# Optimization experiments

Hardware: AMD Instinct MI355X
Metric: run time of the kernel (lower is better)

## Reference

```python
import jax, jax.numpy as jnp
import numpy as np

DIM_M = 512
NEG_INF = -1e30


def setup_inputs() -> dict:
    key = jax.random.key(0)
    k1, k2, k3, k4, k5, k6, k7 = jax.random.split(key, 7)
    B, Lc, Lq, d = 16, 1024, 512, DIM_M
    C = jax.random.normal(k1, (B, Lc, d), dtype=jnp.float32)
    Q = jax.random.normal(k2, (B, Lq, d), dtype=jnp.float32)
    cmask = jax.random.randint(k3, (B, Lc), 0, 2).astype(jnp.float32)
    qmask = jax.random.randint(k4, (B, Lq), 0, 2).astype(jnp.float32)
    lim = np.sqrt(1.0 / d)
    w = jax.random.uniform(k5, (3 * d,), minval=-lim, maxval=lim, dtype=jnp.float32)
    # out_linear: Linear(4d -> d), torch default init
    bound = np.sqrt(1.0 / (4 * d))
    out_w = jax.random.uniform(k6, (d, 4 * d), minval=-bound, maxval=bound, dtype=jnp.float32)
    out_b = jax.random.uniform(k7, (d,), minval=-bound, maxval=bound, dtype=jnp.float32)
    return {"C": C, "Q": Q, "cmask": cmask, "qmask": qmask, "w": w, "out_w": out_w, "out_b": out_b}


def _mask_logits(t, m):
    return t * m + (1.0 - m) * NEG_INF


def reference(C, Q, cmask, qmask, w, out_w, out_b):
    d = C.shape[-1]
    w1, w2, w3 = w[:d], w[d:2 * d], w[2 * d:]
    # Decomposed trilinear similarity (same math as cat([Ct,Qt,Ct*Qt]) @ w):
    # S[b,i,j] = C[b,i]@w1 + Q[b,j]@w2 + (C[b,i]*w3) @ Q[b,j]
    S = (C @ w1)[:, :, None] + (Q @ w2)[:, None, :] \
        + jnp.einsum('bid,bjd->bij', C * w3, Q)  # [B, Lc, Lq]
    qm = qmask[:, None, :]  # [B, 1, Lq]
    cm = cmask[:, :, None]  # [B, Lc, 1]
    S1 = jax.nn.softmax(_mask_logits(S, qm), axis=2)  # over Lq
    S2 = jax.nn.softmax(_mask_logits(S, cm), axis=1)  # over Lc
    A = jnp.einsum('bij,bjd->bid', S1, Q)  # [B, Lc, d]
    # bmm(bmm(S1, S2^T), C) == S1 @ (S2^T @ C) by associativity (cheaper)
    S2TC = jnp.einsum('bij,bid->bjd', S2, C)  # [B, Lq, d]
    Bm = jnp.einsum('bij,bjd->bid', S1, S2TC)  # [B, Lc, d]
    out = jnp.concatenate([C, A, C * A, C * Bm], axis=2)  # [B, Lc, 4d]
    # dropout inactive (inference); out_linear
    return out @ out_w.T + out_b
```

## Files before the change

### kernel.cpp

```cpp
#include <hip/hip_runtime.h>
#include <hip/hip_bf16.h>


#define NB 16
#define LC 1024
#define LQ 512
#define DM 512
#define D4 2048
#define NEGINF (-1e30f)
#define LDA64 72
#define LDA32 40

typedef __bf16 v8bf __attribute__((ext_vector_type(8)));
typedef __bf16 v4bf __attribute__((ext_vector_type(4)));
typedef float  v4f  __attribute__((ext_vector_type(4)));

#define MFMA16 __builtin_amdgcn_mfma_f32_16x16x32_bf16

#define TILE_SETUP8 \
  const int t = threadIdx.x, lane = t & 63, wave = t >> 6; \
  const int wm = wave >> 2, wn = wave & 3, quad = lane >> 4, col = lane & 15; \
  const int sr = t >> 2;

#define ZERO_ACC8 \
  v4f acc[4][2]; \
  _Pragma("unroll") for (int x = 0; x < 4; ++x) \
  _Pragma("unroll") for (int y = 0; y < 2; ++y) \
  _Pragma("unroll") for (int r = 0; r < 4; ++r) acc[x][y][r] = 0.f;

#define FRAG_MMA8S(AL, BL, LDA, KO) do { \
  v8bf af_[4], bf_[2]; \
  _Pragma("unroll") for (int x = 0; x < 4; ++x) \
    af_[x] = *(const v8bf*)&AL[(wm * 64 + x * 16 + col) * LDA + KO + quad * 8]; \
  _Pragma("unroll") for (int y = 0; y < 2; ++y) \
    bf_[y] = *(const v8bf*)&BL[(wn * 32 + y * 16 + col) * LDA + KO + quad * 8]; \
  _Pragma("unroll") for (int x = 0; x < 4; ++x) \
  _Pragma("unroll") for (int y = 0; y < 2; ++y) \
    acc[x][y] = MFMA16(af_[x], bf_[y], acc[x][y], 0, 0, 0); \
} while (0)

__device__ __forceinline__ void xcd_remap(int& bx, int& by, int& bz) {
  const int gx = gridDim.x, gy = gridDim.y, gz = gridDim.z;
  int flat = bx + gx * (by + gy * bz);
  int per = (gx * gy * gz) >> 3;
  int nw = (flat & 7) * per + (flat >> 3);
  bx = nw % gx;
  int r = nw / gx;
  by = r % gy;
  bz = r / gy;
}

__device__ __forceinline__ v8bf cvt8f(float4 a, float4 b) {
  v8bf h;
  h[0] = (__bf16)a.x; h[1] = (__bf16)a.y; h[2] = (__bf16)a.z; h[3] = (__bf16)a.w;
  h[4] = (__bf16)b.x; h[5] = (__bf16)b.y; h[6] = (__bf16)b.z; h[7] = (__bf16)b.w;
  return h;
}

__global__ void k_rowdots(const float* __restrict__ C, const float* __restrict__ Q,
                          const float* __restrict__ w,
                          float* __restrict__ cw1, float* __restrict__ qw2) {
  const int wid = threadIdx.x >> 6, lane = threadIdx.x & 63;
  const int row = blockIdx.x * 4 + wid;
  const bool isC = row < NB * LC;
  const float* src = isC ? (C + (size_t)row * DM) : (Q + (size_t)(row - NB * LC) * DM);
  const float* wv  = isC ? w : (w + DM);
  float v = 0.f;
#pragma unroll
  for (int tt = 0; tt < 8; ++tt) {
    int k = lane + 64 * tt;
    v += src[k] * wv[k];
  }
#pragma unroll
  for (int off = 32; off; off >>= 1) v += __shfl_down(v, off, 64);
  if (lane == 0) {
    if (isC) cw1[row] = v;
    else     qw2[row - NB * LC] = v;
  }
}

__global__ void k_transpose(const float* __restrict__ in, __bf16* __restrict__ outT,
                            int R, int Cd) {
  __shared__ __bf16 tile[64][66];
  const int b = blockIdx.z;
  const int r0 = blockIdx.y * 64, c0 = blockIdx.x * 64;
  const int tr = threadIdx.x >> 6, tc = threadIdx.x & 63;
  const float* inb = in + (size_t)b * R * Cd;
  __bf16* outb = outT + (size_t)b * Cd * R;
  for (int r = tr; r < 64; r += 4)
    tile[r][tc] = (__bf16)inb[(size_t)(r0 + r) * Cd + c0 + tc];
  __syncthreads();
  for (int c = tr; c < 64; c += 4)
    outb[(size_t)(c0 + c) * R + r0 + tc] = tile[tc][c];
}

__global__ void k_owcvt(const float* __restrict__ OW, __bf16* __restrict__ OWb) {
  size_t i = ((size_t)blockIdx.x * 256 + threadIdx.x) * 4;
  float4 f = *(const float4*)(OW + i);
  v4bf h; h[0] = (__bf16)f.x; h[1] = (__bf16)f.y; h[2] = (__bf16)f.z; h[3] = (__bf16)f.w;
  *(v4bf*)(OWb + i) = h;
}

__global__ __launch_bounds__(512) void k_mfma_S(
    const float* __restrict__ C, const float* __restrict__ Q, const float* __restrict__ w,
    const float* __restrict__ cw1, const float* __restrict__ qw2, float* __restrict__ S) {
  __shared__ __bf16 Al[128 * LDA64], Bl[128 * LDA64];
  int bx = blockIdx.x, by = blockIdx.y, bz = blockIdx.z;
  xcd_remap(bx, by, bz);
  const int b = bz, i0 = by * 128, j0 = bx * 128;
  TILE_SETUP8
  const int skc = (t & 3) * 16;
  const float* Cb = C + (size_t)b * LC * DM;
  const float* Qb = Q + (size_t)b * LQ * DM;
  const float* w3 = w + 2 * DM;
  float4 pc[4], pq[4];
  auto load = [&](int k0) {
    const float* ca = Cb + (size_t)(i0 + sr) * DM + k0 + skc;
    const float* qa = Qb + (size_t)(j0 + sr) * DM + k0 + skc;
#pragma unroll
    for (int u = 0; u < 4; ++u) {
      pc[u] = *(const float4*)(ca + 4 * u);
      pq[u] = *(const float4*)(qa + 4 * u);
    }
  };
  load(0);
  ZERO_ACC8
  for (int k0 = 0; k0 < DM; k0 += 64) {
    const float* wa = w3 + k0 + skc;
#pragma unroll
    for (int u = 0; u < 2; ++u) {
      float4 c0 = pc[2 * u], c1 = pc[2 * u + 1];
      float4 w0 = *(const float4*)(wa + 8 * u), w1 = *(const float4*)(wa + 8 * u + 4);
      v8bf ah;
      ah[0] = (__bf16)(c0.x * w0.x); ah[1] = (__bf16)(c0.y * w0.y);
      ah[2] = (__bf16)(c0.z * w0.z); ah[3] = (__bf16)(c0.w * w0.w);
      ah[4] = (__bf16)(c1.x * w1.x); ah[5] = (__bf16)(c1.y * w1.y);
      ah[6] = (__bf16)(c1.z * w1.z); ah[7] = (__bf16)(c1.w * w1.w);
      *(v8bf*)&Al[sr * LDA64 + skc + 8 * u] = ah;
      *(v8bf*)&Bl[sr * LDA64 + skc + 8 * u] = cvt8f(pq[2 * u], pq[2 * u + 1]);
    }
    __syncthreads();
    int kn = k0 + 64; if (kn >= DM) kn = 0;
    load(kn);
    FRAG_MMA8S(Al, Bl, LDA64, 0);
    FRAG_MMA8S(Al, Bl, LDA64, 32);
    __syncthreads();
  }
  float* Sb = S + (size_t)b * LC * LQ;
#pragma unroll
  for (int x = 0; x < 4; ++x) {
    const int mB = i0 + wm * 64 + x * 16 + quad * 4;
    float cv[4];
#pragma unroll
    for (int r = 0; r < 4; ++r) cv[r] = cw1[b * LC + mB + r];
#pragma unroll
    for (int y = 0; y < 2; ++y) {
      const int j = j0 + wn * 32 + y * 16 + col;
      const float qv = qw2[b * LQ + j];
#pragma unroll
      for (int r = 0; r < 4; ++r)
        Sb[(size_t)(mB + r) * LQ + j] = acc[x][y][r] + cv[r] + qv;
    }
  }
}

__global__ __launch_bounds__(1024) void k_softstat(
    const float* __restrict__ S, const float* __restrict__ qmask,
    const float* __restrict__ cmask, __bf16* __restrict__ S1,
    float2* __restrict__ pstat) {
  __shared__ float2 cst[16][LQ];
  const int b = blockIdx.y, ic = blockIdx.x;
  const int tid = threadIdx.x, wv = tid >> 6, lane = tid & 63;
  const float* qm  = qmask + b * LQ;
  const float* cm  = cmask + b * LC + ic * 64;
  const float* Sb  = S  + ((size_t)b * LC + ic * 64) * LQ;
  __bf16*      S1b = S1 + ((size_t)b * LC + ic * 64) * LQ;
  float colm[8], cols[8];
#pragma unroll
  for (int tt = 0; tt < 8; ++tt) { colm[tt] = -3e38f; cols[tt] = 0.f; }
  for (int it = 0; it < 4; ++it) {
    const int r = wv * 4 + it;
    const float cmv = cm[r];
    const float* Srow = Sb + (size_t)r * LQ;
    float sv[8], l1[8];
    float m = -3e38f;
#pragma unroll
    for (int tt = 0; tt < 8; ++tt) {
      int j = lane + 64 * tt;
      sv[tt] = Srow[j];
      float qv = qm[j];
      l1[tt] = qv * sv[tt] + (1.f - qv) * NEGINF;
      m = fmaxf(m, l1[tt]);
    }
#pragma unroll
    for (int off = 32; off; off >>= 1) m = fmaxf(m, __shfl_xor(m, off, 64));
    float e[8], s = 0.f;
#pragma unroll
    for (int tt = 0; tt < 8; ++tt) { e[tt] = __expf(l1[tt] - m); s += e[tt]; }
#pragma unroll
    for (int off = 32; off; off >>= 1) s += __shfl_xor(s, off, 64);
    const float inv = 1.f / s;
#pragma unroll
    for (int tt = 0; tt < 8; ++tt)
      S1b[(size_t)r * LQ + lane + 64 * tt] = (__bf16)(e[tt] * inv);
#pragma unroll
    for (int tt = 0; tt < 8; ++tt) {
      float l2 = cmv * sv[tt] + (1.f - cmv) * NEGINF;
      if (l2 > colm[tt]) { cols[tt] *= __expf(colm[tt] - l2); colm[tt] = l2; }
      cols[tt] += __expf(l2 - colm[tt]);
    }
  }
#pragma unroll
  for (int tt = 0; tt < 8; ++tt) cst[wv][lane + 64 * tt] = make_float2(colm[tt], cols[tt]);
  __syncthreads();
  if (tid < LQ) {
    float M = -3e38f, Sd = 0.f;
#pragma unroll
    for (int k = 0; k < 16; ++k) {
      float2 p = cst[k][tid];
      float nM = fmaxf(M, p.x);
      Sd = Sd * __expf(M - nM) + p.y * __expf(p.x - nM);
      M = nM;
    }
    pstat[((size_t)(b * 16 + ic) * LQ) + tid] = make_float2(M, Sd);
  }
}

__global__ void k_colwrite(const float* __restrict__ S, const float* __restrict__ cmask,
                           const float2* __restrict__ pstat, __bf16* __restrict__ S2T) {
  __shared__ float Mf[64], If[64];
  __shared__ __bf16 tile[64][66];
  const int b = blockIdx.z, ic = blockIdx.y, j0 = blockIdx.x * 64;
  const int c = threadIdx.x & 63, ip = threadIdx.x >> 6;
  if (threadIdx.x < 64) {
    float M = -3e38f, Sd = 0.f;
#pragma unroll
    for (int k = 0; k < 16; ++k) {
      float2 p = pstat[((size_t)(b * 16 + k) * LQ) + j0 + threadIdx.x];
      float nM = fmaxf(M, p.x);
      Sd = Sd * __expf(M - nM) + p.y * __expf(p.x - nM);
      M = nM;
    }
    Mf[threadIdx.x] = M; If[threadIdx.x] = 1.f / Sd;
  }
  __syncthreads();
  const float M = Mf[c], inv = If[c];
  const float* Sb = S + ((size_t)b * LC + ic * 64) * LQ;
  const float* cm = cmask + b * LC + ic * 64;
  for (int r = ip; r < 64; r += 4) {
    float mk = cm[r];
    float logit = mk * Sb[(size_t)r * LQ + j0 + c] + (1.f - mk) * NEGINF;
    tile[r][c] = (__bf16)(__expf(logit - M) * inv);
  }
  __syncthreads();
  __bf16* S2Tb = S2T + ((size_t)b * LQ + j0) * LC + ic * 64;
  for (int jr = ip; jr < 64; jr += 4)
    S2Tb[(size_t)jr * LC + c] = tile[c][jr];
}

__global__ __launch_bounds__(512) void k_mfma_A(
    const __bf16* __restrict__ S1, const __bf16* __restrict__ QT, __bf16* __restrict__ Aw) {
  __shared__ __bf16 Al[128 * LDA64], Bl[128 * LDA64];
  int bx = blockIdx.x, by = blockIdx.y, bz = blockIdx.z;
  xcd_remap(bx, by, bz);
  const int b = bz, i0 = by * 128, n0 = bx * 128;
  TILE_SETUP8
  const int skc = (t & 3) * 16;
  const __bf16* Ar = S1 + (size_t)b * LC * LQ + (size_t)(i0 + sr) * LQ + skc;
  const __bf16* Br = QT + (size_t)b * DM * LQ + (size_t)(n0 + sr) * LQ + skc;
  v8bf pa0, pa1, pb0, pb1;
  auto load = [&](int k0) {
    pa0 = *(const v8bf*)(Ar + k0); pa1 = *(const v8bf*)(Ar + k0 + 8);
    pb0 = *(const v8bf*)(Br + k0); pb1 = *(const v8bf*)(Br + k0 + 8);
  };
  load(0);
  ZERO_ACC8
  for (int k0 = 0; k0 < LQ; k0 += 64) {
    *(v8bf*)&Al[sr * LDA64 + skc] = pa0; *(v8bf*)&Al[sr * LDA64 + skc + 8] = pa1;
    *(v8bf*)&Bl[sr * LDA64 + skc] = pb0; *(v8bf*)&Bl[sr * LDA64 + skc + 8] = pb1;
    __syncthreads();
    int kn = k0 + 64; if (kn >= LQ) kn = 0;
    load(kn);
    FRAG_MMA8S(Al, Bl, LDA64, 0);
    FRAG_MMA8S(Al, Bl, LDA64, 32);
    __syncthreads();
  }
  __bf16* Ab = Aw + (size_t)b * LC * DM;
#pragma unroll
  for (int x = 0; x < 4; ++x) {
    const int mB = i0 + wm * 64 + x * 16 + quad * 4;
#pragma unroll
    for (int y = 0; y < 2; ++y) {
      const int n = n0 + wn * 32 + y * 16 + col;
#pragma unroll
      for (int r = 0; r < 4; ++r)
        Ab[(size_t)(mB + r) * DM + n] = (__bf16)acc[x][y][r];
    }
  }
}

__global__ __launch_bounds__(512) void k_mfma_T(
    const __bf16* __restrict__ S2T, const __bf16* __restrict__ CT, __bf16* __restrict__ S2TCT) {
  __shared__ __bf16 Al[128 * LDA64], Bl[128 * LDA64];
  int bx = blockIdx.x, by = blockIdx.y, bz = blockIdx.z;
  xcd_remap(bx, by, bz);
  const int b = bz, j0 = by * 128, n0 = bx * 128;
  TILE_SETUP8
  const int skc = (t & 3) * 16;
  const __bf16* Ar = S2T + (size_t)b * LQ * LC + (size_t)(j0 + sr) * LC + skc;
  const __bf16* Br = CT  + (size_t)b * DM * LC + (size_t)(n0 + sr) * LC + skc;
  v8bf pa0, pa1, pb0, pb1;
  auto load = [&](int k0) {
    pa0 = *(const v8bf*)(Ar + k0); pa1 = *(const v8bf*)(Ar + k0 + 8);
    pb0 = *(const v8bf*)(Br + k0); pb1 = *(const v8bf*)(Br + k0 + 8);
  };
  load(0);
  ZERO_ACC8
  for (int k0 = 0; k0 < LC; k0 += 64) {
    *(v8bf*)&Al[sr * LDA64 + skc] = pa0; *(v8bf*)&Al[sr * LDA64 + skc + 8] = pa1;
    *(v8bf*)&Bl[sr * LDA64 + skc] = pb0; *(v8bf*)&Bl[sr * LDA64 + skc + 8] = pb1;
    __syncthreads();
    int kn = k0 + 64; if (kn >= LC) kn = 0;
    load(kn);
    FRAG_MMA8S(Al, Bl, LDA64, 0);
    FRAG_MMA8S(Al, Bl, LDA64, 32);
    __syncthreads();
  }
#pragma unroll
  for (int x = 0; x < 4; ++x) {
    const int jB = j0 + wm * 64 + x * 16 + quad * 4;
#pragma unroll
    for (int y = 0; y < 2; ++y) {
      const int n = n0 + wn * 32 + y * 16 + col;
      v4bf h;
#pragma unroll
      for (int r = 0; r < 4; ++r) h[r] = (__bf16)acc[x][y][r];
      *(v4bf*)&S2TCT[((size_t)b * DM + n) * LQ + jB] = h;
    }
  }
}

__global__ __launch_bounds__(512) void k_mfma_Bm(
    const __bf16* __restrict__ S1, const __bf16* __restrict__ S2TCT, __bf16* __restrict__ Bmw) {
  __shared__ __bf16 Al[128 * LDA64], Bl[128 * LDA64];
  int bx = blockIdx.x, by = blockIdx.y, bz = blockIdx.z;
  xcd_remap(bx, by, bz);
  const int b = bz, i0 = by * 128, n0 = bx * 128;
  TILE_SETUP8
  const int skc = (t & 3) * 16;
  const __bf16* Ar = S1    + (size_t)b * LC * LQ + (size_t)(i0 + sr) * LQ + skc;
  const __bf16* Br = S2TCT + (size_t)b * DM * LQ + (size_t)(n0 + sr) * LQ + skc;
  v8bf pa0, pa1, pb0, pb1;
  auto load = [&](int k0) {
    pa0 = *(const v8bf*)(Ar + k0); pa1 = *(const v8bf*)(Ar + k0 + 8);
    pb0 = *(const v8bf*)(Br + k0); pb1 = *(const v8bf*)(Br + k0 + 8);
  };
  load(0);
  ZERO_ACC8
  for (int k0 = 0; k0 < LQ; k0 += 64) {
    *(v8bf*)&Al[sr * LDA64 + skc] = pa0; *(v8bf*)&Al[sr * LDA64 + skc + 8] = pa1;
    *(v8bf*)&Bl[sr * LDA64 + skc] = pb0; *(v8bf*)&Bl[sr * LDA64 + skc + 8] = pb1;
    __syncthreads();
    int kn = k0 + 64; if (kn >= LQ) kn = 0;
    load(kn);
    FRAG_MMA8S(Al, Bl, LDA64, 0);
    FRAG_MMA8S(Al, Bl, LDA64, 32);
    __syncthreads();
  }
  __bf16* Bb = Bmw + (size_t)b * LC * DM;
#pragma unroll
  for (int x = 0; x < 4; ++x) {
    const int mB = i0 + wm * 64 + x * 16 + quad * 4;
#pragma unroll
    for (int y = 0; y < 2; ++y) {
      const int n = n0 + wn * 32 + y * 16 + col;
#pragma unroll
      for (int r = 0; r < 4; ++r)
        Bb[(size_t)(mB + r) * DM + n] = (__bf16)acc[x][y][r];
    }
  }
}

__global__ __launch_bounds__(512) void k_mfma_out(
    const float* __restrict__ C, const __bf16* __restrict__ Aw, const __bf16* __restrict__ Bmw,
    const __bf16* __restrict__ OWb, const float* __restrict__ ob, float* __restrict__ out) {
  __shared__ __bf16 Asg[4][128 * LDA32], Bsg[4][128 * LDA32];
  int bx = blockIdx.x, by = blockIdx.y, bz = blockIdx.z;
  xcd_remap(bx, by, bz);
  const int b = bz, i0 = by * 128, n0 = bx * 128;
  TILE_SETUP8
  const int skc = (t & 3) * 8;
  const float*  Cr = C   + (size_t)b * LC * DM + (size_t)(i0 + sr) * DM + skc;
  const __bf16* Ar = Aw  + (size_t)b * LC * DM + (size_t)(i0 + sr) * DM + skc;
  const __bf16* Br = Bmw + (size_t)b * LC * DM + (size_t)(i0 + sr) * DM + skc;
  const __bf16* Wr = OWb + (size_t)(n0 + sr) * D4 + skc;
  float4 pc0, pc1; v8bf pA, pB, pw[4];
  auto load = [&](int kl) {
    pc0 = *(const float4*)(Cr + kl); pc1 = *(const float4*)(Cr + kl + 4);
    pA = *(const v8bf*)(Ar + kl);
    pB = *(const v8bf*)(Br + kl);
#pragma unroll
    for (int s = 0; s < 4; ++s) pw[s] = *(const v8bf*)(Wr + s * DM + kl);
  };
  load(0);
  ZERO_ACC8
  for (int kl = 0; kl < DM; kl += 32) {
    float cf[8] = {pc0.x, pc0.y, pc0.z, pc0.w, pc1.x, pc1.y, pc1.z, pc1.w};
    v8bf hC, hCA, hCB;
#pragma unroll
    for (int e = 0; e < 8; ++e) {
      hC[e]  = (__bf16)cf[e];
      hCA[e] = (__bf16)(cf[e] * (float)pA[e]);
      hCB[e] = (__bf16)(cf[e] * (float)pB[e]);
    }
    const int off = sr * LDA32 + skc;
    *(v8bf*)&Asg[0][off] = hC;
    *(v8bf*)&Asg[1][off] = pA;
    *(v8bf*)&Asg[2][off] = hCA;
    *(v8bf*)&Asg[3][off] = hCB;
#pragma unroll
    for (int s = 0; s < 4; ++s) *(v8bf*)&Bsg[s][off] = pw[s];
    __syncthreads();
    int kn = kl + 32; if (kn >= DM) kn = 0;
    load(kn);
#pragma unroll
    for (int s = 0; s < 4; ++s) FRAG_MMA8S(Asg[s], Bsg[s], LDA32, 0);
    __syncthreads();
  }
  float* outb = out + (size_t)b * LC * DM;
#pragma unroll
  for (int x = 0; x < 4; ++x) {
    const int mB = i0 + wm * 64 + x * 16 + quad * 4;
#pragma unroll
    for (int y = 0; y < 2; ++y) {
      const int n = n0 + wn * 32 + y * 16 + col;
      const float bv = ob[n];
#pragma unroll
      for (int r = 0; r < 4; ++r)
        outb[(size_t)(mB + r) * DM + n] = acc[x][y][r] + bv;
    }
  }
}

extern "C" void kernel_launch(void* const* d_in, const int* in_sizes, int n_in,
                              void* d_out, int out_size, void* d_ws, size_t ws_size,
                              hipStream_t stream) {
  const float* C     = (const float*)d_in[0];
  const float* Q     = (const float*)d_in[1];
  const float* cmask = (const float*)d_in[2];
  const float* qmask = (const float*)d_in[3];
  const float* w     = (const float*)d_in[4];
  const float* out_w = (const float*)d_in[5];
  const float* out_b = (const float*)d_in[6];
  float* out = (float*)d_out;

  char* base = (char*)d_ws;
  float*  cw1   = (float*)base;
  float*  qw2   = (float*)(base + 65536);
  char*   R     = base + 131072;
  float*  S     = (float*)R;
  __bf16* Aw    = (__bf16*)R;
  __bf16* CT    = (__bf16*)(R + (16u << 20));
  __bf16* Bmw   = (__bf16*)(R + (16u << 20));
  __bf16* S1    = (__bf16*)(base + 131072 + (32u << 20));
  __bf16* S2T   = (__bf16*)(base + 131072 + (48u << 20));
  __bf16* OWbf  = S2T;
  char*   Z     = base + 131072 + (64u << 20);
  float2* pstat = (float2*)Z;
  __bf16* QT    = (__bf16*)Z;
  __bf16* S2TCT = (__bf16*)Z;
  (void)in_sizes; (void)n_in; (void)out_size; (void)ws_size;

  k_rowdots<<<(NB * LC + NB * LQ) / 4, 256, 0, stream>>>(C, Q, w, cw1, qw2);
  k_mfma_S<<<dim3(LQ / 128, LC / 128, NB), 512, 0, stream>>>(C, Q, w, cw1, qw2, S);
  k_softstat<<<dim3(LC / 64, NB), 1024, 0, stream>>>(S, qmask, cmask, S1, pstat);
  k_colwrite<<<dim3(LQ / 64, LC / 64, NB), 256, 0, stream>>>(S, cmask, pstat, S2T);
  k_transpose<<<dim3(DM / 64, LQ / 64, NB), 256, 0, stream>>>(Q, QT, LQ, DM);
  k_transpose<<<dim3(DM / 64, LC / 64, NB), 256, 0, stream>>>(C, CT, LC, DM);
  k_mfma_A<<<dim3(DM / 128, LC / 128, NB), 512, 0, stream>>>(S1, QT, Aw);
  k_mfma_T<<<dim3(DM / 128, LQ / 128, NB), 512, 0, stream>>>(S2T, CT, S2TCT);
  k_owcvt<<<DM * D4 / 1024, 256, 0, stream>>>(out_w, OWbf);
  k_mfma_Bm<<<dim3(DM / 128, LC / 128, NB), 512, 0, stream>>>(S1, S2TCT, Bmw);
  k_mfma_out<<<dim3(DM / 128, LC / 128, NB), 512, 0, stream>>>(C, Aw, Bmw, OWbf, out_b, out);
}
```

Baseline: 281.1 us.

## Fuse row dots into S GEMM, vectorize softmax/transpose, use 4-wave 64x64 warp tiles

Removes the separate row-dot kernel by computing C·w1 and Q·w2 inside the S GEMM's load loop and reducing them through shared memory. Vectorizes global loads and stores in softstat, colwrite and transpose (float4 reads, packed bf16 writes). Switches the A, Bm and output GEMMs from 8 waves with 64x32 per-wave tiles to 4 waves with 64x64 per-wave tiles, which raises register use per thread and changes occupancy. The fused dot products add redundant w1/w2 loads per block of the S GEMM.

```diff
diff --git a/kernel.cpp b/kernel.cpp
--- a/kernel.cpp
+++ b/kernel.cpp
@@ -19,8 +19,7 @@
 
 #define TILE_SETUP8 \
   const int t = threadIdx.x, lane = t & 63, wave = t >> 6; \
-  const int wm = wave >> 2, wn = wave & 3, quad = lane >> 4, col = lane & 15; \
-  const int sr = t >> 2;
+  const int wm = wave >> 2, wn = wave & 3, quad = lane >> 4, col = lane & 15;
 
 #define ZERO_ACC8 \
   v4f acc[4][2]; \
@@ -39,6 +38,27 @@
     acc[x][y] = MFMA16(af_[x], bf_[y], acc[x][y], 0, 0, 0); \
 } while (0)
 
+#define TILE_SETUP4 \
+  const int t = threadIdx.x, lane = t & 63, wave = t >> 6; \
+  const int wm = wave >> 1, wn = wave & 1, quad = lane >> 4, col = lane & 15;
+
+#define ZERO_ACC4 \
+  v4f acc[4][4]; \
+  _Pragma("unroll") for (int x = 0; x < 4; ++x) \
+  _Pragma("unroll") for (int y = 0; y < 4; ++y) \
+  _Pragma("unroll") for (int r = 0; r < 4; ++r) acc[x][y][r] = 0.f;
+
+#define FRAG_MMA4(AL, BL, LDA, KO) do { \
+  v8bf af_[4], bf_[4]; \
+  _Pragma("unroll") for (int x = 0; x < 4; ++x) \
+    af_[x] = *(const v8bf*)&AL[(wm * 64 + x * 16 + col) * LDA + KO + quad * 8]; \
+  _Pragma("unroll") for (int y = 0; y < 4; ++y) \
+    bf_[y] = *(const v8bf*)&BL[(wn * 64 + y * 16 + col) * LDA + KO + quad * 8]; \
+  _Pragma("unroll") for (int x = 0; x < 4; ++x) \
+  _Pragma("unroll") for (int y = 0; y < 4; ++y) \
+    acc[x][y] = MFMA16(af_[x], bf_[y], acc[x][y], 0, 0, 0); \
+} while (0)
+
 __device__ __forceinline__ void xcd_remap(int& bx, int& by, int& bz) {
   const int gx = gridDim.x, gy = gridDim.y, gz = gridDim.z;
   int flat = bx + gx * (by + gy * bz);
@@ -57,41 +77,31 @@
   return h;
 }
 
-__global__ void k_rowdots(const float* __restrict__ C, const float* __restrict__ Q,
-                          const float* __restrict__ w,
-                          float* __restrict__ cw1, float* __restrict__ qw2) {
-  const int wid = threadIdx.x >> 6, lane = threadIdx.x & 63;
-  const int row = blockIdx.x * 4 + wid;
-  const bool isC = row < NB * LC;
-  const float* src = isC ? (C + (size_t)row * DM) : (Q + (size_t)(row - NB * LC) * DM);
-  const float* wv  = isC ? w : (w + DM);
-  float v = 0.f;
-#pragma unroll
-  for (int tt = 0; tt < 8; ++tt) {
-    int k = lane + 64 * tt;
-    v += src[k] * wv[k];
-  }
-#pragma unroll
-  for (int off = 32; off; off >>= 1) v += __shfl_down(v, off, 64);
-  if (lane == 0) {
-    if (isC) cw1[row] = v;
-    else     qw2[row - NB * LC] = v;
-  }
-}
-
 __global__ void k_transpose(const float* __restrict__ in, __bf16* __restrict__ outT,
                             int R, int Cd) {
   __shared__ __bf16 tile[64][66];
   const int b = blockIdx.z;
   const int r0 = blockIdx.y * 64, c0 = blockIdx.x * 64;
-  const int tr = threadIdx.x >> 6, tc = threadIdx.x & 63;
   const float* inb = in + (size_t)b * R * Cd;
   __bf16* outb = outT + (size_t)b * Cd * R;
-  for (int r = tr; r < 64; r += 4)
-    tile[r][tc] = (__bf16)inb[(size_t)(r0 + r) * Cd + c0 + tc];
+  const int rr = threadIdx.x >> 4, c4 = (threadIdx.x & 15) * 4;
+#pragma unroll
+  for (int p = 0; p < 4; ++p) {
+    const int r = rr + p * 16;
+    float4 f = *(const float4*)(inb + (size_t)(r0 + r) * Cd + c0 + c4);
+    tile[r][c4 + 0] = (__bf16)f.x; tile[r][c4 + 1] = (__bf16)f.y;
+    tile[r][c4 + 2] = (__bf16)f.z; tile[r][c4 + 3] = (__bf16)f.w;
+  }
   __syncthreads();
-  for (int c = tr; c < 64; c += 4)
-    outb[(size_t)(c0 + c) * R + r0 + tc] = tile[tc][c];
+  const int c = threadIdx.x & 63, rb = (threadIdx.x >> 6) * 4;
+#pragma unroll
+  for (int p = 0; p < 4; ++p) {
+    const int r4 = rb + p * 16;
+    v4bf h;
+#pragma unroll
+    for (int e = 0; e < 4; ++e) h[e] = tile[r4 + e][c];
+    *(v4bf*)(outb + (size_t)(c0 + c) * R + r0 + r4) = h;
+  }
 }
 
 __global__ void k_owcvt(const float* __restrict__ OW, __bf16* __restrict__ OWb) {
@@ -103,16 +113,17 @@
 
 __global__ __launch_bounds__(512) void k_mfma_S(
     const float* __restrict__ C, const float* __restrict__ Q, const float* __restrict__ w,
-    const float* __restrict__ cw1, const float* __restrict__ qw2, float* __restrict__ S) {
+    float* __restrict__ S) {
   __shared__ __bf16 Al[128 * LDA64], Bl[128 * LDA64];
+  __shared__ float cwL[128], qwL[128];
   int bx = blockIdx.x, by = blockIdx.y, bz = blockIdx.z;
   xcd_remap(bx, by, bz);
   const int b = bz, i0 = by * 128, j0 = bx * 128;
   TILE_SETUP8
-  const int skc = (t & 3) * 16;
+  const int sr = t >> 2, skc = (t & 3) * 16;
   const float* Cb = C + (size_t)b * LC * DM;
   const float* Qb = Q + (size_t)b * LQ * DM;
-  const float* w3 = w + 2 * DM;
+  const float* w1 = w, *w2 = w + DM, *w3 = w + 2 * DM;
   float4 pc[4], pq[4];
   auto load = [&](int k0) {
     const float* ca = Cb + (size_t)(i0 + sr) * DM + k0 + skc;
@@ -125,19 +136,29 @@
   };
   load(0);
   ZERO_ACC8
+  float cdot = 0.f, qdot = 0.f;
   for (int k0 = 0; k0 < DM; k0 += 64) {
-    const float* wa = w3 + k0 + skc;
 #pragma unroll
     for (int u = 0; u < 2; ++u) {
       float4 c0 = pc[2 * u], c1 = pc[2 * u + 1];
-      float4 w0 = *(const float4*)(wa + 8 * u), w1 = *(const float4*)(wa + 8 * u + 4);
+      float4 q0 = pq[2 * u], q1 = pq[2 * u + 1];
+      const float* w3a = w3 + k0 + skc + 8 * u;
+      float4 w30 = *(const float4*)w3a, w31 = *(const float4*)(w3a + 4);
+      const float* w1a = w1 + k0 + skc + 8 * u;
+      float4 w10 = *(const float4*)w1a, w11 = *(const float4*)(w1a + 4);
+      const float* w2a = w2 + k0 + skc + 8 * u;
+      float4 w20 = *(const float4*)w2a, w21 = *(const float4*)(w2a + 4);
       v8bf ah;
-      ah[0] = (__bf16)(c0.x * w0.x); ah[1] = (__bf16)(c0.y * w0.y);
-      ah[2] = (__bf16)(c0.z * w0.z); ah[3] = (__bf16)(c0.w * w0.w);
-      ah[4] = (__bf16)(c1.x * w1.x); ah[5] = (__bf16)(c1.y * w1.y);
-      ah[6] = (__bf16)(c1.z * w1.z); ah[7] = (__bf16)(c1.w * w1.w);
+      ah[0] = (__bf16)(c0.x * w30.x); ah[1] = (__bf16)(c0.y * w30.y);
+      ah[2] = (__bf16)(c0.z * w30.z); ah[3] = (__bf16)(c0.w * w30.w);
+      ah[4] = (__bf16)(c1.x * w31.x); ah[5] = (__bf16)(c1.y * w31.y);
+      ah[6] = (__bf16)(c1.z * w31.z); ah[7] = (__bf16)(c1.w * w31.w);
       *(v8bf*)&Al[sr * LDA64 + skc + 8 * u] = ah;
-      *(v8bf*)&Bl[sr * LDA64 + skc + 8 * u] = cvt8f(pq[2 * u], pq[2 * u + 1]);
+      *(v8bf*)&Bl[sr * LDA64 + skc + 8 * u] = cvt8f(q0, q1);
+      cdot += c0.x * w10.x + c0.y * w10.y + c0.z * w10.z + c0.w * w10.w
+            + c1.x * w11.x + c1.y * w11.y + c1.z * w11.z + c1.w * w11.w;
+      qdot += q0.x * w20.x + q0.y * w20.y + q0.z * w20.z + q0.w * w20.w
+            + q1.x * w21.x + q1.y * w21.y + q1.z * w21.z + q1.w * w21.w;
     }
     __syncthreads();
     int kn = k0 + 64; if (kn >= DM) kn = 0;
@@ -146,20 +167,24 @@
     FRAG_MMA8S(Al, Bl, LDA64, 32);
     __syncthreads();
   }
+  cdot += __shfl_xor(cdot, 1); cdot += __shfl_xor(cdot, 2);
+  qdot += __shfl_xor(qdot, 1); qdot += __shfl_xor(qdot, 2);
+  if ((t & 3) == 0) { cwL[sr] = cdot; qwL[sr] = qdot; }
+  __syncthreads();
   float* Sb = S + (size_t)b * LC * LQ;
 #pragma unroll
   for (int x = 0; x < 4; ++x) {
-    const int mB = i0 + wm * 64 + x * 16 + quad * 4;
+    const int ml = wm * 64 + x * 16 + quad * 4;
     float cv[4];
 #pragma unroll
-    for (int r = 0; r < 4; ++r) cv[r] = cw1[b * LC + mB + r];
+    for (int r = 0; r < 4; ++r) cv[r] = cwL[ml + r];
 #pragma unroll
     for (int y = 0; y < 2; ++y) {
-      const int j = j0 + wn * 32 + y * 16 + col;
-      const float qv = qw2[b * LQ + j];
+      const int jl = wn * 32 + y * 16 + col;
+      const float qv = qwL[jl];
 #pragma unroll
       for (int r = 0; r < 4; ++r)
-        Sb[(size_t)(mB + r) * LQ + j] = acc[x][y][r] + cv[r] + qv;
+        Sb[(size_t)(i0 + ml + r) * LQ + j0 + jl] = acc[x][y][r] + cv[r] + qv;
     }
   }
 }
@@ -171,47 +196,54 @@
   __shared__ float2 cst[16][LQ];
   const int b = blockIdx.y, ic = blockIdx.x;
   const int tid = threadIdx.x, wv = tid >> 6, lane = tid & 63;
+  const int jb = lane * 8;
   const float* qm  = qmask + b * LQ;
   const float* cm  = cmask + b * LC + ic * 64;
   const float* Sb  = S  + ((size_t)b * LC + ic * 64) * LQ;
   __bf16*      S1b = S1 + ((size_t)b * LC + ic * 64) * LQ;
+  float qv[8];
+  {
+    float4 q0 = *(const float4*)(qm + jb), q1 = *(const float4*)(qm + jb + 4);
+    qv[0] = q0.x; qv[1] = q0.y; qv[2] = q0.z; qv[3] = q0.w;
+    qv[4] = q1.x; qv[5] = q1.y; qv[6] = q1.z; qv[7] = q1.w;
+  }
   float colm[8], cols[8];
 #pragma unroll
-  for (int tt = 0; tt < 8; ++tt) { colm[tt] = -3e38f; cols[tt] = 0.f; }
+  for (int e = 0; e < 8; ++e) { colm[e] = -3e38f; cols[e] = 0.f; }
   for (int it = 0; it < 4; ++it) {
     const int r = wv * 4 + it;
     const float cmv = cm[r];
-    const float* Srow = Sb + (size_t)r * LQ;
-    float sv[8], l1[8];
+    const float* Srow = Sb + (size_t)r * LQ + jb;
+    float4 s0 = *(const float4*)Srow, s1 = *(const float4*)(Srow + 4);
+    float sv[8] = {s0.x, s0.y, s0.z, s0.w, s1.x, s1.y, s1.z, s1.w};
+    float l1[8];
     float m = -3e38f;
 #pragma unroll
-    for (int tt = 0; tt < 8; ++tt) {
-      int j = lane + 64 * tt;
-      sv[tt] = Srow[j];
-      float qv = qm[j];
-      l1[tt] = qv * sv[tt] + (1.f - qv) * NEGINF;
-      m = fmaxf(m, l1[tt]);
+    for (int e = 0; e < 8; ++e) {
+      l1[e] = qv[e] * sv[e] + (1.f - qv[e]) * NEGINF;
+      m = fmaxf(m, l1[e]);
     }
 #pragma unroll
     for (int off = 32; off; off >>= 1) m = fmaxf(m, __shfl_xor(m, off, 64));
-    float e[8], s = 0.f;
-#pragma unroll
-    for (int tt = 0; tt < 8; ++tt) { e[tt] = __expf(l1[tt] - m); s += e[tt]; }
+    float ex[8], s = 0.f;
+#pragma unroll
+    for (int e = 0; e < 8; ++e) { ex[e] = __expf(l1[e] - m); s += ex[e]; }
 #pragma unroll
     for (int off = 32; off; off >>= 1) s += __shfl_xor(s, off, 64);
     const float inv = 1.f / s;
-#pragma unroll
-    for (int tt = 0; tt < 8; ++tt)
-      S1b[(size_t)r * LQ + lane + 64 * tt] = (__bf16)(e[tt] * inv);
-#pragma unroll
-    for (int tt = 0; tt < 8; ++tt) {
-      float l2 = cmv * sv[tt] + (1.f - cmv) * NEGINF;
-      if (l2 > colm[tt]) { cols[tt] *= __expf(colm[tt] - l2); colm[tt] = l2; }
-      cols[tt] += __expf(l2 - colm[tt]);
-    }
-  }
-#pragma unroll
-  for (int tt = 0; tt < 8; ++tt) cst[wv][lane + 64 * tt] = make_float2(colm[tt], cols[tt]);
+    v8bf h;
+#pragma unroll
+    for (int e = 0; e < 8; ++e) h[e] = (__bf16)(ex[e] * inv);
+    *(v8bf*)(S1b + (size_t)r * LQ + jb) = h;
+#pragma unroll
+    for (int e = 0; e < 8; ++e) {
+      float l2 = cmv * sv[e] + (1.f - cmv) * NEGINF;
+      if (l2 > colm[e]) { cols[e] *= __expf(colm[e] - l2); colm[e] = l2; }
+      cols[e] += __expf(l2 - colm[e]);
+    }
+  }
+#pragma unroll
+  for (int e = 0; e < 8; ++e) cst[wv][jb + e] = make_float2(colm[e], cols[e]);
   __syncthreads();
   if (tid < LQ) {
     float M = -3e38f, Sd = 0.f;
@@ -231,7 +263,6 @@
   __shared__ float Mf[64], If[64];
   __shared__ __bf16 tile[64][66];
   const int b = blockIdx.z, ic = blockIdx.y, j0 = blockIdx.x * 64;
-  const int c = threadIdx.x & 63, ip = threadIdx.x >> 6;
   if (threadIdx.x < 64) {
     float M = -3e38f, Sd = 0.f;
 #pragma unroll
@@ -244,45 +275,65 @@
     Mf[threadIdx.x] = M; If[threadIdx.x] = 1.f / Sd;
   }
   __syncthreads();
-  const float M = Mf[c], inv = If[c];
   const float* Sb = S + ((size_t)b * LC + ic * 64) * LQ;
   const float* cm = cmask + b * LC + ic * 64;
-  for (int r = ip; r < 64; r += 4) {
-    float mk = cm[r];
-    float logit = mk * Sb[(size_t)r * LQ + j0 + c] + (1.f - mk) * NEGINF;
-    tile[r][c] = (__bf16)(__expf(logit - M) * inv);
+  const int rr = threadIdx.x >> 4, c4 = (threadIdx.x & 15) * 4;
+#pragma unroll
+  for (int p = 0; p < 4; ++p) {
+    const int r = rr + p * 16;
+    const float mk = cm[r];
+    float4 sv = *(const float4*)(Sb + (size_t)r * LQ + j0 + c4);
+    float s[4] = {sv.x, sv.y, sv.z, sv.w};
+#pragma unroll
+    for (int e = 0; e < 4; ++e) {
+      float logit = mk * s[e] + (1.f - mk) * NEGINF;
+      tile[r][c4 + e] = (__bf16)(__expf(logit - Mf[c4 + e]) * If[c4 + e]);
+    }
   }
   __syncthreads();
   __bf16* S2Tb = S2T + ((size_t)b * LQ + j0) * LC + ic * 64;
-  for (int jr = ip; jr < 64; jr += 4)
-    S2Tb[(size_t)jr * LC + c] = tile[c][jr];
-}
-
-__global__ __launch_bounds__(512) void k_mfma_A(
+  const int c = threadIdx.x & 63, rb = (threadIdx.x >> 6) * 4;
+#pragma unroll
+  for (int p = 0; p < 4; ++p) {
+    const int r4 = rb + p * 16;
+    v4bf h;
+#pragma unroll
+    for (int e = 0; e < 4; ++e) h[e] = tile[r4 + e][c];
+    *(v4bf*)(S2Tb + (size_t)c * LC + r4) = h;
+  }
+}
+
+__global__ __launch_bounds__(256) void k_mfma_A(
     const __bf16* __restrict__ S1, const __bf16* __restrict__ QT, __bf16* __restrict__ Aw) {
   __shared__ __bf16 Al[128 * LDA64], Bl[128 * LDA64];
   int bx = blockIdx.x, by = blockIdx.y, bz = blockIdx.z;
   xcd_remap(bx, by, bz);
   const int b = bz, i0 = by * 128, n0 = bx * 128;
-  TILE_SETUP8
-  const int skc = (t & 3) * 16;
-  const __bf16* Ar = S1 + (size_t)b * LC * LQ + (size_t)(i0 + sr) * LQ + skc;
-  const __bf16* Br = QT + (size_t)b * DM * LQ + (size_t)(n0 + sr) * LQ + skc;
-  v8bf pa0, pa1, pb0, pb1;
+  TILE_SETUP4
+  const int sr = t >> 1, kh = (t & 1) * 32;
+  const __bf16* Ar = S1 + (size_t)b * LC * LQ + (size_t)(i0 + sr) * LQ + kh;
+  const __bf16* Br = QT + (size_t)b * DM * LQ + (size_t)(n0 + sr) * LQ + kh;
+  v8bf pa[4], pb[4];
   auto load = [&](int k0) {
-    pa0 = *(const v8bf*)(Ar + k0); pa1 = *(const v8bf*)(Ar + k0 + 8);
-    pb0 = *(const v8bf*)(Br + k0); pb1 = *(const v8bf*)(Br + k0 + 8);
+#pragma unroll
+    for (int u = 0; u < 4; ++u) {
+      pa[u] = *(const v8bf*)(Ar + k0 + 8 * u);
+      pb[u] = *(const v8bf*)(Br + k0 + 8 * u);
+    }
   };
   load(0);
-  ZERO_ACC8
+  ZERO_ACC4
   for (int k0 = 0; k0 < LQ; k0 += 64) {
-    *(v8bf*)&Al[sr * LDA64 + skc] = pa0; *(v8bf*)&Al[sr * LDA64 + skc + 8] = pa1;
-    *(v8bf*)&Bl[sr * LDA64 + skc] = pb0; *(v8bf*)&Bl[sr * LDA64 + skc + 8] = pb1;
+#pragma unroll
+    for (int u = 0; u < 4; ++u) {
+      *(v8bf*)&Al[sr * LDA64 + kh + 8 * u] = pa[u];
+      *(v8bf*)&Bl[sr * LDA64 + kh + 8 * u] = pb[u];
+    }
     __syncthreads();
     int kn = k0 + 64; if (kn >= LQ) kn = 0;
     load(kn);
-    FRAG_MMA8S(Al, Bl, LDA64, 0);
-    FRAG_MMA8S(Al, Bl, LDA64, 32);
+    FRAG_MMA4(Al, Bl, LDA64, 0);
+    FRAG_MMA4(Al, Bl, LDA64, 32);
     __syncthreads();
   }
   __bf16* Ab = Aw + (size_t)b * LC * DM;
@@ -290,8 +341,8 @@
   for (int x = 0; x < 4; ++x) {
     const int mB = i0 + wm * 64 + x * 16 + quad * 4;
 #pragma unroll
-    for (int y = 0; y < 2; ++y) {
-      const int n = n0 + wn * 32 + y * 16 + col;
+    for (int y = 0; y < 4; ++y) {
+      const int n = n0 + wn * 64 + y * 16 + col;
 #pragma unroll
       for (int r = 0; r < 4; ++r)
         Ab[(size_t)(mB + r) * DM + n] = (__bf16)acc[x][y][r];
@@ -306,7 +357,7 @@
   xcd_remap(bx, by, bz);
   const int b = bz, j0 = by * 128, n0 = bx * 128;
   TILE_SETUP8
-  const int skc = (t & 3) * 16;
+  const int sr = t >> 2, skc = (t & 3) * 16;
   const __bf16* Ar = S2T + (size_t)b * LQ * LC + (size_t)(j0 + sr) * LC + skc;
   const __bf16* Br = CT  + (size_t)b * DM * LC + (size_t)(n0 + sr) * LC + skc;
   v8bf pa0, pa1, pb0, pb1;
@@ -340,31 +391,37 @@
   }
 }
 
-__global__ __launch_bounds__(512) void k_mfma_Bm(
+__global__ __launch_bounds__(256) void k_mfma_Bm(
     const __bf16* __restrict__ S1, const __bf16* __restrict__ S2TCT, __bf16* __restrict__ Bmw) {
   __shared__ __bf16 Al[128 * LDA64], Bl[128 * LDA64];
   int bx = blockIdx.x, by = blockIdx.y, bz = blockIdx.z;
   xcd_remap(bx, by, bz);
   const int b = bz, i0 = by * 128, n0 = bx * 128;
-  TILE_SETUP8
-  const int skc = (t & 3) * 16;
-  const __bf16* Ar = S1    + (size_t)b * LC * LQ + (size_t)(i0 + sr) * LQ + skc;
-  const __bf16* Br = S2TCT + (size_t)b * DM * LQ + (size_t)(n0 + sr) * LQ + skc;
-  v8bf pa0, pa1, pb0, pb1;
+  TILE_SETUP4
+  const int sr = t >> 1, kh = (t & 1) * 32;
+  const __bf16* Ar = S1    + (size_t)b * LC * LQ + (size_t)(i0 + sr) * LQ + kh;
+  const __bf16* Br = S2TCT + (size_t)b * DM * LQ + (size_t)(n0 + sr) * LQ + kh;
+  v8bf pa[4], pb[4];
   auto load = [&](int k0) {
-    pa0 = *(const v8bf*)(Ar + k0); pa1 = *(const v8bf*)(Ar + k0 + 8);
-    pb0 = *(const v8bf*)(Br + k0); pb1 = *(const v8bf*)(Br + k0 + 8);
+#pragma unroll
+    for (int u = 0; u < 4; ++u) {
+      pa[u] = *(const v8bf*)(Ar + k0 + 8 * u);
+      pb[u] = *(const v8bf*)(Br + k0 + 8 * u);
+    }
   };
   load(0);
-  ZERO_ACC8
+  ZERO_ACC4
   for (int k0 = 0; k0 < LQ; k0 += 64) {
-    *(v8bf*)&Al[sr * LDA64 + skc] = pa0; *(v8bf*)&Al[sr * LDA64 + skc + 8] = pa1;
-    *(v8bf*)&Bl[sr * LDA64 + skc] = pb0; *(v8bf*)&Bl[sr * LDA64 + skc + 8] = pb1;
+#pragma unroll
+    for (int u = 0; u < 4; ++u) {
+      *(v8bf*)&Al[sr * LDA64 + kh + 8 * u] = pa[u];
+      *(v8bf*)&Bl[sr * LDA64 + kh + 8 * u] = pb[u];
+    }
     __syncthreads();
     int kn = k0 + 64; if (kn >= LQ) kn = 0;
     load(kn);
-    FRAG_MMA8S(Al, Bl, LDA64, 0);
-    FRAG_MMA8S(Al, Bl, LDA64, 32);
+    FRAG_MMA4(Al, Bl, LDA64, 0);
+    FRAG_MMA4(Al, Bl, LDA64, 32);
     __syncthreads();
   }
   __bf16* Bb = Bmw + (size_t)b * LC * DM;
@@ -372,8 +429,8 @@
   for (int x = 0; x < 4; ++x) {
     const int mB = i0 + wm * 64 + x * 16 + quad * 4;
 #pragma unroll
-    for (int y = 0; y < 2; ++y) {
-      const int n = n0 + wn * 32 + y * 16 + col;
+    for (int y = 0; y < 4; ++y) {
+      const int n = n0 + wn * 64 + y * 16 + col;
 #pragma unroll
       for (int r = 0; r < 4; ++r)
         Bb[(size_t)(mB + r) * DM + n] = (__bf16)acc[x][y][r];
@@ -381,50 +438,60 @@
   }
 }
 
-__global__ __launch_bounds__(512) void k_mfma_out(
+__global__ __launch_bounds__(256) void k_mfma_out(
     const float* __restrict__ C, const __bf16* __restrict__ Aw, const __bf16* __restrict__ Bmw,
     const __bf16* __restrict__ OWb, const float* __restrict__ ob, float* __restrict__ out) {
   __shared__ __bf16 Asg[4][128 * LDA32], Bsg[4][128 * LDA32];
   int bx = blockIdx.x, by = blockIdx.y, bz = blockIdx.z;
   xcd_remap(bx, by, bz);
   const int b = bz, i0 = by * 128, n0 = bx * 128;
-  TILE_SETUP8
-  const int skc = (t & 3) * 8;
-  const float*  Cr = C   + (size_t)b * LC * DM + (size_t)(i0 + sr) * DM + skc;
-  const __bf16* Ar = Aw  + (size_t)b * LC * DM + (size_t)(i0 + sr) * DM + skc;
-  const __bf16* Br = Bmw + (size_t)b * LC * DM + (size_t)(i0 + sr) * DM + skc;
-  const __bf16* Wr = OWb + (size_t)(n0 + sr) * D4 + skc;
-  float4 pc0, pc1; v8bf pA, pB, pw[4];
+  TILE_SETUP4
+  const int sr = t >> 1, kh = (t & 1) * 16;
+  const float*  Cr = C   + (size_t)b * LC * DM + (size_t)(i0 + sr) * DM + kh;
+  const __bf16* Ar = Aw  + (size_t)b * LC * DM + (size_t)(i0 + sr) * DM + kh;
+  const __bf16* Br = Bmw + (size_t)b * LC * DM + (size_t)(i0 + sr) * DM + kh;
+  const __bf16* Wr = OWb + (size_t)(n0 + sr) * D4 + kh;
+  float4 pc[4]; v8bf pA[2], pB[2], pw[4][2];
   auto load = [&](int kl) {
-    pc0 = *(const float4*)(Cr + kl); pc1 = *(const float4*)(Cr + kl + 4);
-    pA = *(const v8bf*)(Ar + kl);
-    pB = *(const v8bf*)(Br + kl);
-#pragma unroll
-    for (int s = 0; s < 4; ++s) pw[s] = *(const v8bf*)(Wr + s * DM + kl);
+#pragma unroll
+    for (int u = 0; u < 4; ++u) pc[u] = *(const float4*)(Cr + kl + 4 * u);
+#pragma unroll
+    for (int u = 0; u < 2; ++u) {
+      pA[u] = *(const v8bf*)(Ar + kl + 8 * u);
+      pB[u] = *(const v8bf*)(Br + kl + 8 * u);
+    }
+#pragma unroll
+    for (int s = 0; s < 4; ++s)
+#pragma unroll
+      for (int u = 0; u < 2; ++u) pw[s][u] = *(const v8bf*)(Wr + s * DM + kl + 8 * u);
   };
   load(0);
-  ZERO_ACC8
+  ZERO_ACC4
   for (int kl = 0; kl < DM; kl += 32) {
-    float cf[8] = {pc0.x, pc0.y, pc0.z, pc0.w, pc1.x, pc1.y, pc1.z, pc1.w};
-    v8bf hC, hCA, hCB;
-#pragma unroll
-    for (int e = 0; e < 8; ++e) {
-      hC[e]  = (__bf16)cf[e];
-      hCA[e] = (__bf16)(cf[e] * (float)pA[e]);
-      hCB[e] = (__bf16)(cf[e] * (float)pB[e]);
-    }
-    const int off = sr * LDA32 + skc;
-    *(v8bf*)&Asg[0][off] = hC;
-    *(v8bf*)&Asg[1][off] = pA;
-    *(v8bf*)&Asg[2][off] = hCA;
-    *(v8bf*)&Asg[3][off] = hCB;
-#pragma unroll
-    for (int s = 0; s < 4; ++s) *(v8bf*)&Bsg[s][off] = pw[s];
+#pragma unroll
+    for (int u = 0; u < 2; ++u) {
+      float4 f0 = pc[2 * u], f1 = pc[2 * u + 1];
+      float cf[8] = {f0.x, f0.y, f0.z, f0.w, f1.x, f1.y, f1.z, f1.w};
+      v8bf hC, hCA, hCB;
+#pragma unroll
+      for (int e = 0; e < 8; ++e) {
+        hC[e]  = (__bf16)cf[e];
+        hCA[e] = (__bf16)(cf[e] * (float)pA[u][e]);
+        hCB[e] = (__bf16)(cf[e] * (float)pB[u][e]);
+      }
+      const int off = sr * LDA32 + kh + 8 * u;
+      *(v8bf*)&Asg[0][off] = hC;
+      *(v8bf*)&Asg[1][off] = pA[u];
+      *(v8bf*)&Asg[2][off] = hCA;
+      *(v8bf*)&Asg[3][off] = hCB;
+#pragma unroll
+      for (int s = 0; s < 4; ++s) *(v8bf*)&Bsg[s][off] = pw[s][u];
+    }
     __syncthreads();
     int kn = kl + 32; if (kn >= DM) kn = 0;
     load(kn);
 #pragma unroll
-    for (int s = 0; s < 4; ++s) FRAG_MMA8S(Asg[s], Bsg[s], LDA32, 0);
+    for (int s = 0; s < 4; ++s) FRAG_MMA4(Asg[s], Bsg[s], LDA32, 0);
     __syncthreads();
   }
   float* outb = out + (size_t)b * LC * DM;
@@ -432,8 +499,8 @@
   for (int x = 0; x < 4; ++x) {
     const int mB = i0 + wm * 64 + x * 16 + quad * 4;
 #pragma unroll
-    for (int y = 0; y < 2; ++y) {
-      const int n = n0 + wn * 32 + y * 16 + col;
+    for (int y = 0; y < 4; ++y) {
+      const int n = n0 + wn * 64 + y * 16 + col;
       const float bv = ob[n];
 #pragma unroll
       for (int r = 0; r < 4; ++r)
@@ -455,8 +522,6 @@
   float* out = (float*)d_out;
 
   char* base = (char*)d_ws;
-  float*  cw1   = (float*)base;
-  float*  qw2   = (float*)(base + 65536);
   char*   R     = base + 131072;
   float*  S     = (float*)R;
   __bf16* Aw    = (__bf16*)R;
@@ -471,15 +536,14 @@
   __bf16* S2TCT = (__bf16*)Z;
   (void)in_sizes; (void)n_in; (void)out_size; (void)ws_size;
 
-  k_rowdots<<<(NB * LC + NB * LQ) / 4, 256, 0, stream>>>(C, Q, w, cw1, qw2);
-  k_mfma_S<<<dim3(LQ / 128, LC / 128, NB), 512, 0, stream>>>(C, Q, w, cw1, qw2, S);
+  k_mfma_S<<<dim3(LQ / 128, LC / 128, NB), 512, 0, stream>>>(C, Q, w, S);
   k_softstat<<<dim3(LC / 64, NB), 1024, 0, stream>>>(S, qmask, cmask, S1, pstat);
   k_colwrite<<<dim3(LQ / 64, LC / 64, NB), 256, 0, stream>>>(S, cmask, pstat, S2T);
   k_transpose<<<dim3(DM / 64, LQ / 64, NB), 256, 0, stream>>>(Q, QT, LQ, DM);
   k_transpose<<<dim3(DM / 64, LC / 64, NB), 256, 0, stream>>>(C, CT, LC, DM);
-  k_mfma_A<<<dim3(DM / 128, LC / 128, NB), 512, 0, stream>>>(S1, QT, Aw);
+  k_mfma_A<<<dim3(DM / 128, LC / 128, NB), 256, 0, stream>>>(S1, QT, Aw);
   k_mfma_T<<<dim3(DM / 128, LQ / 128, NB), 512, 0, stream>>>(S2T, CT, S2TCT);
   k_owcvt<<<DM * D4 / 1024, 256, 0, stream>>>(out_w, OWbf);
-  k_mfma_Bm<<<dim3(DM / 128, LC / 128, NB), 512, 0, stream>>>(S1, S2TCT, Bmw);
-  k_mfma_out<<<dim3(DM / 128, LC / 128, NB), 512, 0, stream>>>(C, Aw, Bmw, OWbf, out_b, out);
-}
+  k_mfma_Bm<<<dim3(DM / 128, LC / 128, NB), 256, 0, stream>>>(S1, S2TCT, Bmw);
+  k_mfma_out<<<dim3(DM / 128, LC / 128, NB), 256, 0, stream>>>(C, Aw, Bmw, OWbf, out_b, out);
+}
```

New measurement: 315.5 us. +12.2%, slower.
